# Kernel optimization log

Hardware: AMD Instinct MI355X
Metric: run time of the kernel (lower is better)

## Reference

```python
import jax, jax.numpy as jnp
import numpy as np

EPS = 1e-5

def _conv1x1(x, w, b):
    # x: (b,c,t,h,w), w: (o,c), b: (o,)  -> (b,o,t,h,w)
    return jnp.einsum('bcthw,oc->bothw', x, w) + b[None, :, None, None, None]

def setup_inputs() -> dict:
    key = jax.random.key(0)
    ks = jax.random.split(key, 12)
    B, C, IC, T, H, W = 32, 1024, 512, 8, 16, 8
    s_c = 1.0 / np.sqrt(C)
    s_ic = 1.0 / np.sqrt(IC)
    return {
        'x':       jax.random.normal(ks[0], (B, C, T, H, W), jnp.float32),
        'g_w':     jax.random.normal(ks[1], (IC, C), jnp.float32) * s_c,
        'g_b':     jax.random.normal(ks[2], (IC,), jnp.float32) * 0.01,
        'theta_w': jax.random.normal(ks[3], (IC, C), jnp.float32) * s_c,
        'theta_b': jax.random.normal(ks[4], (IC,), jnp.float32) * 0.01,
        'phi_w':   jax.random.normal(ks[5], (IC, C), jnp.float32) * s_c,
        'phi_b':   jax.random.normal(ks[6], (IC,), jnp.float32) * 0.01,
        'w_w':     jax.random.normal(ks[7], (C, IC), jnp.float32) * s_ic,
        'w_b':     jax.random.normal(ks[8], (C,), jnp.float32) * 0.01,
        'bn_gamma': jax.random.normal(ks[9], (C,), jnp.float32) * 0.1 + 1.0,
        'bn_beta':  jax.random.normal(ks[10], (C,), jnp.float32) * 0.01,
        'bn_mean':  jax.random.normal(ks[11], (C,), jnp.float32) * 0.01,
        'bn_var':   jnp.ones((C,), jnp.float32),
    }

def reference(x, g_w, g_b, theta_w, theta_b, phi_w, phi_b, w_w, w_b,
              bn_gamma, bn_beta, bn_mean, bn_var):
    B, C, T, H, W = x.shape
    IC = g_w.shape[0]
    # value projection, flattened per frame: (b, t, ic*h*w)
    g_x = _conv1x1(x, g_w, g_b)                       # (b,ic,t,h,w)
    g_x = jnp.transpose(g_x, (0, 2, 1, 3, 4)).reshape(B, T, IC * H * W)
    # pooled query/key over spatial dims: (b,t,ic) and (b,ic,t)
    theta = _conv1x1(x, theta_w, theta_b).mean(axis=(3, 4))   # (b,ic,t)
    phi = _conv1x1(x, phi_w, phi_b).mean(axis=(3, 4))         # (b,ic,t)
    f = jnp.einsum('bct,bcs->bts', theta, phi)                # (b,t,t)
    attn = jax.nn.softmax(f, axis=-1)
    y = jnp.einsum('bts,bsd->btd', attn, g_x)                 # (b,t,ic*h*w)
    y = jnp.transpose(y.reshape(B, T, IC, H, W), (0, 2, 1, 3, 4))  # (b,ic,t,h,w)
    # output projection + BatchNorm3d (inference stats) + residual
    wy = _conv1x1(y, w_w, w_b)                        # (b,c,t,h,w)
    inv = bn_gamma / jnp.sqrt(bn_var + EPS)
    wy = wy * inv[None, :, None, None, None] + (bn_beta - bn_mean * inv)[None, :, None, None, None]
    return wy + x
```

## Files before the change

kernel.cpp:

```cpp
#include <hip/hip_runtime.h>
#include <hip/hip_bf16.h>

typedef __attribute__((ext_vector_type(8))) short bf16x8;
typedef __attribute__((ext_vector_type(4))) float f32x4;

__global__ __launch_bounds__(256) void pool_kernel(const float* __restrict__ x,
                                                   float* __restrict__ xbar) {
    int row = blockIdx.x * 16 + (threadIdx.x >> 4);
    int j = threadIdx.x & 15;
    const float4* p = (const float4*)(x + (size_t)row * 128);
    float4 a = p[j * 2], b2 = p[j * 2 + 1];
    float s = a.x + a.y + a.z + a.w + b2.x + b2.y + b2.z + b2.w;
    s += __shfl_xor(s, 1); s += __shfl_xor(s, 2);
    s += __shfl_xor(s, 4); s += __shfl_xor(s, 8);
    if (j == 0) xbar[row] = s * (1.0f / 128.0f);
}

__global__ __launch_bounds__(256) void thetaphi_kernel(
        const float* __restrict__ xbar,
        const float* __restrict__ tw, const float* __restrict__ tb,
        const float* __restrict__ pw, const float* __restrict__ pb,
        float* __restrict__ theta, float* __restrict__ phi) {
    int which = blockIdx.x & 1;
    int icc = (blockIdx.x >> 1) & 15;
    int b = blockIdx.x >> 5;
    const float* w = which ? pw : tw;
    const float* bias = which ? pb : tb;
    float* out = which ? phi : theta;
    __shared__ float xs[8192];
    for (int i = threadIdx.x; i < 8192; i += 256) xs[i] = xbar[b * 8192 + i];
    __syncthreads();
    int icl = threadIdx.x >> 3;
    int t = threadIdx.x & 7;
    int ic = icc * 32 + icl;
    const float* wr = w + (size_t)ic * 1024;
    float acc = 0.0f;
    #pragma unroll 8
    for (int k = 0; k < 1024; k++) acc += wr[k] * xs[k * 8 + t];
    out[((size_t)b * 512 + ic) * 8 + t] = acc + bias[ic];
}

__global__ __launch_bounds__(64) void attn_kernel(const float* __restrict__ theta,
                                                  const float* __restrict__ phi,
                                                  float* __restrict__ attn) {
    __shared__ float th[4096], ph[4096];
    int b = blockIdx.x, lane = threadIdx.x;
    for (int i = lane; i < 4096; i += 64) {
        th[i] = theta[(size_t)b * 4096 + i];
        ph[i] = phi[(size_t)b * 4096 + i];
    }
    __syncthreads();
    int t = lane >> 3, s = lane & 7;
    float f = 0.0f;
    #pragma unroll 8
    for (int ic = 0; ic < 512; ic++) f += th[ic * 8 + t] * ph[ic * 8 + s];
    float m = f;
    m = fmaxf(m, __shfl_xor(m, 1));
    m = fmaxf(m, __shfl_xor(m, 2));
    m = fmaxf(m, __shfl_xor(m, 4));
    float e = __expf(f - m);
    float sum = e;
    sum += __shfl_xor(sum, 1); sum += __shfl_xor(sum, 2); sum += __shfl_xor(sum, 4);
    attn[b * 64 + lane] = e / sum;
}

__global__ __launch_bounds__(256) void prep_operands_kernel(
        const float* __restrict__ gw, const float* __restrict__ ww,
        __hip_bfloat16* __restrict__ gwt, __hip_bfloat16* __restrict__ wwb) {
    int bid = blockIdx.x;
    if (bid < 512) {
        int icb = bid >> 5;
        int cb = bid & 31;
        __shared__ float tile[32][33];
        int r = threadIdx.x >> 5, c = threadIdx.x & 31;
        #pragma unroll
        for (int i = 0; i < 4; i++)
            tile[r + i * 8][c] = gw[(size_t)(icb * 32 + r + i * 8) * 1024 + cb * 32 + c];
        __syncthreads();
        #pragma unroll
        for (int i = 0; i < 4; i++) {
            int cin = cb * 32 + r + i * 8;
            gwt[(size_t)cin * 512 + icb * 32 + c] = __float2bfloat16(tile[c][r + i * 8]);
        }
    } else {
        int b2 = bid - 512;
        size_t base = (size_t)b2 * 2048 + (size_t)threadIdx.x * 8;
        const float4* src = (const float4*)(ww + base);
        float4 v0 = src[0], v1 = src[1];
        __hip_bfloat16 tmp[8];
        tmp[0] = __float2bfloat16(v0.x); tmp[1] = __float2bfloat16(v0.y);
        tmp[2] = __float2bfloat16(v0.z); tmp[3] = __float2bfloat16(v0.w);
        tmp[4] = __float2bfloat16(v1.x); tmp[5] = __float2bfloat16(v1.y);
        tmp[6] = __float2bfloat16(v1.z); tmp[7] = __float2bfloat16(v1.w);
        *(bf16x8*)(wwb + base) = *(const bf16x8*)tmp;
    }
}

#if defined(__has_builtin)
#if __has_builtin(__builtin_amdgcn_global_load_lds)
#define USE_GLOAD_LDS 1
#endif
#endif

__device__ __forceinline__ void gload_lds16(const void* g, void* ldsbase) {
#ifdef USE_GLOAD_LDS
    __builtin_amdgcn_global_load_lds(
        (__attribute__((address_space(1))) void*)(g),
        (__attribute__((address_space(3))) void*)(ldsbase), 16, 0, 0);
#endif
}

__global__ __launch_bounds__(256) void prepM_mfma_kernel(
        const __hip_bfloat16* __restrict__ wwb,
        const __hip_bfloat16* __restrict__ gwt,
        __hip_bfloat16* __restrict__ M) {
    __shared__ __align__(16) __hip_bfloat16 As[128 * 32];
    __shared__ __align__(16) __hip_bfloat16 Bs[128 * 32];
    int bid = blockIdx.x;
    int mb = bid >> 3, nb = bid & 7;
    int c0 = mb * 128, n0 = nb * 128;
    int tid = threadIdx.x;
    int w = tid >> 6, l = tid & 63;
    int wr = w >> 1, wc = w & 1;
    const __hip_bfloat16* Ab = wwb + (size_t)c0 * 512;
    const __hip_bfloat16* Bb = gwt + (size_t)n0 * 512;
    int arow = tid >> 2, akq = tid & 3;
    f32x4 acc[4][4] = {};

    for (int kk = 0; kk < 16; ++kk) {
        int k0 = kk * 32;
#ifdef USE_GLOAD_LDS
        gload_lds16(Ab + (size_t)arow * 512 + k0 + akq * 8,        (char*)As + w * 1024);
        gload_lds16(Ab + (size_t)(arow + 64) * 512 + k0 + akq * 8, (char*)As + 4096 + w * 1024);
        gload_lds16(Bb + (size_t)arow * 512 + k0 + akq * 8,        (char*)Bs + w * 1024);
        gload_lds16(Bb + (size_t)(arow + 64) * 512 + k0 + akq * 8, (char*)Bs + 4096 + w * 1024);
#else
        *(bf16x8*)((char*)As + (size_t)tid * 16)        = *(const bf16x8*)(Ab + (size_t)arow * 512 + k0 + akq * 8);
        *(bf16x8*)((char*)As + 4096 + (size_t)tid * 16) = *(const bf16x8*)(Ab + (size_t)(arow + 64) * 512 + k0 + akq * 8);
        *(bf16x8*)((char*)Bs + (size_t)tid * 16)        = *(const bf16x8*)(Bb + (size_t)arow * 512 + k0 + akq * 8);
        *(bf16x8*)((char*)Bs + 4096 + (size_t)tid * 16) = *(const bf16x8*)(Bb + (size_t)(arow + 64) * 512 + k0 + akq * 8);
#endif
        __syncthreads();
        const __hip_bfloat16* Ap = As + ((size_t)(wr * 64 + (l & 15)) * 32) + (l >> 4) * 8;
        const __hip_bfloat16* Bp = Bs + ((size_t)(wc * 64 + (l & 15)) * 32) + (l >> 4) * 8;
        bf16x8 af[4], bfr[4];
        #pragma unroll
        for (int m = 0; m < 4; m++) af[m] = *(const bf16x8*)(Ap + m * 16 * 32);
        #pragma unroll
        for (int n = 0; n < 4; n++) bfr[n] = *(const bf16x8*)(Bp + n * 16 * 32);
        #pragma unroll
        for (int m = 0; m < 4; m++)
            #pragma unroll
            for (int n = 0; n < 4; n++)
                acc[m][n] = __builtin_amdgcn_mfma_f32_16x16x32_bf16(af[m], bfr[n], acc[m][n], 0, 0, 0);
        __syncthreads();
    }

    int col = l & 15, rg = l >> 4;
    #pragma unroll
    for (int m = 0; m < 4; m++)
        #pragma unroll
        for (int j = 0; j < 4; j++) {
            int gc = c0 + wr * 64 + m * 16 + rg * 4 + j;
            #pragma unroll
            for (int n = 0; n < 4; n++)
                M[(size_t)gc * 1024 + n0 + wc * 64 + n * 16 + col] = __float2bfloat16(acc[m][n][j]);
        }
}

__global__ __launch_bounds__(256) void prepbias_kernel(
        const float* __restrict__ ww, const float* __restrict__ gb,
        const float* __restrict__ wb, const float* __restrict__ gamma,
        const float* __restrict__ beta, const float* __restrict__ mean,
        const float* __restrict__ var, float* __restrict__ inv,
        float* __restrict__ shift) {
    int wv = threadIdx.x >> 6, l = threadIdx.x & 63;
    int c = blockIdx.x * 32 + wv * 8 + (l >> 3);
    int j = l & 7;
    const float* wr = ww + (size_t)c * 512;
    float acc = 0.0f;
    #pragma unroll 8
    for (int k = j; k < 512; k += 8) acc += wr[k] * gb[k];
    acc += __shfl_xor(acc, 1); acc += __shfl_xor(acc, 2); acc += __shfl_xor(acc, 4);
    if (j == 0) {
        float cb = wb[c] + acc;
        float iv = gamma[c] * rsqrtf(var[c] + 1e-5f);
        inv[c] = iv;
        shift[c] = cb * iv + beta[c] - mean[c] * iv;
    }
}

__global__ __launch_bounds__(256) void mix_kernel(const float* __restrict__ x,
                                                  const float* __restrict__ attn,
                                                  __hip_bfloat16* __restrict__ xmt) {
    int orig = blockIdx.x;
    int wg = (orig & 7) * 64 + (orig >> 3);
    int b = wg >> 4;
    int hwg = wg & 15;
    __shared__ float at[64];
    __shared__ float xs[8][8][33];
    int tid = threadIdx.x;
    if (tid < 64) at[tid] = attn[b * 64 + tid];
    int ci = tid >> 3, s = tid & 7;
    int h = tid >> 5, cq = tid & 31;
    const float* xb = x + ((size_t)b << 20);
    __hip_bfloat16* ob = xmt + ((size_t)b << 20);
    for (int cc = 0; cc < 32; ++cc) {
        const float4* src = (const float4*)(xb + ((size_t)(cc * 32 + ci) * 8 + s) * 128 + hwg * 8);
        float4 v0 = src[0], v1 = src[1];
        __syncthreads();
        xs[s][0][ci] = v0.x; xs[s][1][ci] = v0.y; xs[s][2][ci] = v0.z; xs[s][3][ci] = v0.w;
        xs[s][4][ci] = v1.x; xs[s][5][ci] = v1.y; xs[s][6][ci] = v1.z; xs[s][7][ci] = v1.w;
        __syncthreads();
        float xr[8];
        #pragma unroll
        for (int ss = 0; ss < 8; ss++) xr[ss] = xs[ss][h][cq];
        #pragma unroll
        for (int t = 0; t < 8; t++) {
            float o = 0.0f;
            #pragma unroll
            for (int ss = 0; ss < 8; ss++) o += at[t * 8 + ss] * xr[ss];
            ob[(size_t)(t * 128 + hwg * 8 + h) * 1024 + cc * 32 + cq] = __float2bfloat16(o);
        }
    }
}

__global__ __launch_bounds__(512, 2) void gemm256_kernel(
        const __hip_bfloat16* __restrict__ Mw,
        const __hip_bfloat16* __restrict__ xmt,
        const float* __restrict__ x,
        const float* __restrict__ inv, const float* __restrict__ shift,
        float* __restrict__ out) {
    __shared__ __align__(16) __hip_bfloat16 HBs[65536];
    char* AH = (char*)HBs;
    const int BUFB = 32768;

    int orig = blockIdx.x;
    int bid = (orig & 7) * 64 + (orig >> 3);
    int b = bid >> 4;
    int mb = (bid >> 2) & 3;
    int nb = bid & 3;
    int c0 = mb * 256, n0 = nb * 256;

    int tid = threadIdx.x;
    int w = tid >> 6, l = tid & 63;
    int wr = w >> 2, wc = w & 3;

    int sgl = (((l & 3) - ((l >> 3) & 3)) & 3);
    const __hip_bfloat16* aS = Mw + (size_t)(c0 + w * 16 + (l >> 2)) * 1024 + sgl * 8;
    const __hip_bfloat16* bS = xmt + ((size_t)b << 20) + (size_t)(n0 + w * 16 + (l >> 2)) * 1024 + sgl * 8;
    int stBase = w * 1024;

    int rdSlot = ((l >> 4) + (((l & 15) >> 1) & 3)) & 3;
    int aRdBase = (wr * 128 + (l & 15)) * 64 + rdSlot * 16;
    int bRdBase = 16384 + (wc * 64 + (l & 15)) * 64 + rdSlot * 16;

    f32x4 acc[8][4] = {};

    #define ISSUE(q3) do {                                                      \
        gload_lds16(aS,              AH + (q3) * BUFB + stBase);                \
        gload_lds16(aS + 128 * 1024, AH + (q3) * BUFB + stBase + 8192);         \
        gload_lds16(bS,              AH + (q3) * BUFB + 16384 + stBase);        \
        gload_lds16(bS + 128 * 1024, AH + (q3) * BUFB + 16384 + stBase + 8192); \
        aS += 32; bS += 32;                                                     \
    } while (0)

    #define V8 asm volatile("s_waitcnt vmcnt(8)" ::: "memory")
    #define V4 asm volatile("s_waitcnt vmcnt(4)" ::: "memory")
    #define V0 asm volatile("s_waitcnt vmcnt(0)" ::: "memory")

    #define HSTEP(q, DOISS, WAITM, LAST) do {                                   \
        if (DOISS) ISSUE(((q) + 3) & 3);                                        \
        const char* bufA = AH + (q) * BUFB;                                     \
        bf16x8 bfr[4];                                                          \
        _Pragma("unroll")                                                       \
        for (int n = 0; n < 4; ++n)                                             \
            bfr[n] = *(const bf16x8*)(bufA + bRdBase + n * 1024);               \
        __builtin_amdgcn_s_setprio(1);                                          \
        _Pragma("unroll")                                                       \
        for (int mi = 0; mi < 8; ++mi) {                                        \
            bf16x8 af = *(const bf16x8*)(bufA + aRdBase + mi * 1024);           \
            _Pragma("unroll")                                                   \
            for (int n = 0; n < 4; ++n)                                         \
                acc[mi][n] = __builtin_amdgcn_mfma_f32_16x16x32_bf16(           \
                    af, bfr[n], acc[mi][n], 0, 0, 0);                           \
        }                                                                       \
        __builtin_amdgcn_s_setprio(0);                                          \
        if (!LAST) {                                                            \
            WAITM;                                                              \
            __builtin_amdgcn_s_barrier();                                       \
            __builtin_amdgcn_sched_barrier(0);                                  \
        }                                                                       \
    } while (0)

    ISSUE(0); ISSUE(1); ISSUE(2);
    V8;
    __builtin_amdgcn_s_barrier();
    __builtin_amdgcn_sched_barrier(0);

    #pragma unroll 1
    for (int t = 0; t < 7; ++t) {
        HSTEP(0, 1, V8, 0);
        HSTEP(1, 1, V8, 0);
        HSTEP(2, 1, V8, 0);
        HSTEP(3, 1, V8, 0);
    }
    HSTEP(0, 1, V8, 0);
    HSTEP(1, 0, V4, 0);
    HSTEP(2, 0, V0, 0);
    HSTEP(3, 0, V0, 1);

    #undef ISSUE
    #undef HSTEP
    #undef V8
    #undef V4
    #undef V0

    int col = l & 15, rg = l >> 4;
    const float* xb = x + ((size_t)b << 20);
    float* ob = out + ((size_t)b << 20);
    #pragma unroll
    for (int mi = 0; mi < 8; ++mi) {
        #pragma unroll
        for (int j = 0; j < 4; ++j) {
            int gc = c0 + wr * 128 + mi * 16 + rg * 4 + j;
            float iv = inv[gc], sh = shift[gc];
            size_t rowoff = (size_t)gc * 1024 + n0 + wc * 64 + col;
            #pragma unroll
            for (int n = 0; n < 4; ++n) {
                size_t idx = rowoff + n * 16;
                ob[idx] = acc[mi][n][j] * iv + sh + xb[idx];
            }
        }
    }
}

extern "C" void kernel_launch(void* const* d_in, const int* in_sizes, int n_in,
                              void* d_out, int out_size, void* d_ws, size_t ws_size,
                              hipStream_t stream) {
    const float* x    = (const float*)d_in[0];
    const float* g_w  = (const float*)d_in[1];
    const float* g_b  = (const float*)d_in[2];
    const float* th_w = (const float*)d_in[3];
    const float* th_b = (const float*)d_in[4];
    const float* ph_w = (const float*)d_in[5];
    const float* ph_b = (const float*)d_in[6];
    const float* w_w  = (const float*)d_in[7];
    const float* w_b  = (const float*)d_in[8];
    const float* gam  = (const float*)d_in[9];
    const float* bet  = (const float*)d_in[10];
    const float* mea  = (const float*)d_in[11];
    const float* var  = (const float*)d_in[12];
    float* out = (float*)d_out;
    char* ws = (char*)d_ws;

    __hip_bfloat16* xmt = (__hip_bfloat16*)ws;
    __hip_bfloat16* Mw  = (__hip_bfloat16*)(ws + 67108864);
    float* xbar  = (float*)(ws + 69206016);
    float* theta = (float*)(ws + 70254592);
    float* phi   = (float*)(ws + 70778880);
    float* attn  = (float*)(ws + 71303168);
    float* inv   = (float*)(ws + 71311360);
    float* shift = (float*)(ws + 71315456);
    __hip_bfloat16* gwt = (__hip_bfloat16*)ws;
    __hip_bfloat16* wwb = (__hip_bfloat16*)(ws + 1048576);

    hipLaunchKernelGGL(pool_kernel, dim3(16384), dim3(256), 0, stream, x, xbar);
    hipLaunchKernelGGL(thetaphi_kernel, dim3(1024), dim3(256), 0, stream,
                       xbar, th_w, th_b, ph_w, ph_b, theta, phi);
    hipLaunchKernelGGL(attn_kernel, dim3(32), dim3(64), 0, stream, theta, phi, attn);
    hipLaunchKernelGGL(prep_operands_kernel, dim3(768), dim3(256), 0, stream,
                       g_w, w_w, gwt, wwb);
    hipLaunchKernelGGL(prepM_mfma_kernel, dim3(64), dim3(256), 0, stream, wwb, gwt, Mw);
    hipLaunchKernelGGL(prepbias_kernel, dim3(32), dim3(256), 0, stream,
                       w_w, g_b, w_b, gam, bet, mea, var, inv, shift);
    hipLaunchKernelGGL(mix_kernel, dim3(512), dim3(256), 0, stream, x, attn, xmt);
    hipLaunchKernelGGL(gemm256_kernel, dim3(512), dim3(512), 0, stream,
                       Mw, xmt, x, inv, shift, out);
}
```

Baseline: 238.2 us.

## Merge independent prep kernels into two combined launches by block-index dispatch

Combines pooling, weight transpose/convert, and bias prep into one early kernel, and the theta/phi projection with the M-weight MFMA GEMM into a second kernel, dispatching on block index. This cuts the launch count from eight to five and lets independent small stages run concurrently on the GPU instead of back to back. The trade-off is larger, uniform shared memory (32 KB) for all blocks of the second kernel, which could lower occupancy for the theta/phi blocks.

```diff
diff --git a/kernel.cpp b/kernel.cpp
--- a/kernel.cpp
+++ b/kernel.cpp
@@ -4,40 +4,163 @@
 typedef __attribute__((ext_vector_type(8))) short bf16x8;
 typedef __attribute__((ext_vector_type(4))) float f32x4;
 
-__global__ __launch_bounds__(256) void pool_kernel(const float* __restrict__ x,
-                                                   float* __restrict__ xbar) {
-    int row = blockIdx.x * 16 + (threadIdx.x >> 4);
-    int j = threadIdx.x & 15;
-    const float4* p = (const float4*)(x + (size_t)row * 128);
-    float4 a = p[j * 2], b2 = p[j * 2 + 1];
-    float s = a.x + a.y + a.z + a.w + b2.x + b2.y + b2.z + b2.w;
-    s += __shfl_xor(s, 1); s += __shfl_xor(s, 2);
-    s += __shfl_xor(s, 4); s += __shfl_xor(s, 8);
-    if (j == 0) xbar[row] = s * (1.0f / 128.0f);
-}
-
-__global__ __launch_bounds__(256) void thetaphi_kernel(
+#if defined(__has_builtin)
+#if __has_builtin(__builtin_amdgcn_global_load_lds)
+#define USE_GLOAD_LDS 1
+#endif
+#endif
+
+__device__ __forceinline__ void gload_lds16(const void* g, void* ldsbase) {
+#ifdef USE_GLOAD_LDS
+    __builtin_amdgcn_global_load_lds(
+        (__attribute__((address_space(1))) void*)(g),
+        (__attribute__((address_space(3))) void*)(ldsbase), 16, 0, 0);
+#endif
+}
+
+__global__ __launch_bounds__(256) void early_kernel(
+        const float* __restrict__ x, float* __restrict__ xbar,
+        const float* __restrict__ gw, const float* __restrict__ ww,
+        __hip_bfloat16* __restrict__ gwt, __hip_bfloat16* __restrict__ wwb,
+        const float* __restrict__ gb, const float* __restrict__ wb,
+        const float* __restrict__ gamma, const float* __restrict__ beta,
+        const float* __restrict__ mean, const float* __restrict__ var,
+        float* __restrict__ inv, float* __restrict__ shift) {
+    __shared__ float tile[32][33];
+    int bid = blockIdx.x;
+    int tid = threadIdx.x;
+    if (bid < 16384) {
+        int row = bid * 16 + (tid >> 4);
+        int j = tid & 15;
+        const float4* p = (const float4*)(x + (size_t)row * 128);
+        float4 a = p[j * 2], b2 = p[j * 2 + 1];
+        float s = a.x + a.y + a.z + a.w + b2.x + b2.y + b2.z + b2.w;
+        s += __shfl_xor(s, 1); s += __shfl_xor(s, 2);
+        s += __shfl_xor(s, 4); s += __shfl_xor(s, 8);
+        if (j == 0) xbar[row] = s * (1.0f / 128.0f);
+    } else if (bid < 16896) {
+        int b2 = bid - 16384;
+        int icb = b2 >> 5, cb = b2 & 31;
+        int r = tid >> 5, c = tid & 31;
+        #pragma unroll
+        for (int i = 0; i < 4; i++)
+            tile[r + i * 8][c] = gw[(size_t)(icb * 32 + r + i * 8) * 1024 + cb * 32 + c];
+        __syncthreads();
+        #pragma unroll
+        for (int i = 0; i < 4; i++) {
+            int cin = cb * 32 + r + i * 8;
+            gwt[(size_t)cin * 512 + icb * 32 + c] = __float2bfloat16(tile[c][r + i * 8]);
+        }
+    } else if (bid < 17152) {
+        int b2 = bid - 16896;
+        size_t base = (size_t)b2 * 2048 + (size_t)tid * 8;
+        const float4* src = (const float4*)(ww + base);
+        float4 v0 = src[0], v1 = src[1];
+        __hip_bfloat16 tmp[8];
+        tmp[0] = __float2bfloat16(v0.x); tmp[1] = __float2bfloat16(v0.y);
+        tmp[2] = __float2bfloat16(v0.z); tmp[3] = __float2bfloat16(v0.w);
+        tmp[4] = __float2bfloat16(v1.x); tmp[5] = __float2bfloat16(v1.y);
+        tmp[6] = __float2bfloat16(v1.z); tmp[7] = __float2bfloat16(v1.w);
+        *(bf16x8*)(wwb + base) = *(const bf16x8*)tmp;
+    } else {
+        int b2 = bid - 17152;
+        int wv = tid >> 6, l = tid & 63;
+        int c = b2 * 32 + wv * 8 + (l >> 3);
+        int j = l & 7;
+        const float* wr = ww + (size_t)c * 512;
+        float acc = 0.0f;
+        #pragma unroll 8
+        for (int k = j; k < 512; k += 8) acc += wr[k] * gb[k];
+        acc += __shfl_xor(acc, 1); acc += __shfl_xor(acc, 2); acc += __shfl_xor(acc, 4);
+        if (j == 0) {
+            float cb2 = wb[c] + acc;
+            float iv = gamma[c] * rsqrtf(var[c] + 1e-5f);
+            inv[c] = iv;
+            shift[c] = cb2 * iv + beta[c] - mean[c] * iv;
+        }
+    }
+}
+
+__global__ __launch_bounds__(256) void stage2_kernel(
         const float* __restrict__ xbar,
         const float* __restrict__ tw, const float* __restrict__ tb,
         const float* __restrict__ pw, const float* __restrict__ pb,
-        float* __restrict__ theta, float* __restrict__ phi) {
-    int which = blockIdx.x & 1;
-    int icc = (blockIdx.x >> 1) & 15;
-    int b = blockIdx.x >> 5;
-    const float* w = which ? pw : tw;
-    const float* bias = which ? pb : tb;
-    float* out = which ? phi : theta;
-    __shared__ float xs[8192];
-    for (int i = threadIdx.x; i < 8192; i += 256) xs[i] = xbar[b * 8192 + i];
-    __syncthreads();
-    int icl = threadIdx.x >> 3;
-    int t = threadIdx.x & 7;
-    int ic = icc * 32 + icl;
-    const float* wr = w + (size_t)ic * 1024;
-    float acc = 0.0f;
-    #pragma unroll 8
-    for (int k = 0; k < 1024; k++) acc += wr[k] * xs[k * 8 + t];
-    out[((size_t)b * 512 + ic) * 8 + t] = acc + bias[ic];
+        float* __restrict__ theta, float* __restrict__ phi,
+        const __hip_bfloat16* __restrict__ wwb,
+        const __hip_bfloat16* __restrict__ gwt,
+        __hip_bfloat16* __restrict__ M) {
+    __shared__ __align__(16) char smem[32768];
+    int bid = blockIdx.x;
+    int tid = threadIdx.x;
+    if (bid < 1024) {
+        float* xs = (float*)smem;
+        int which = bid & 1;
+        int icc = (bid >> 1) & 15;
+        int b = bid >> 5;
+        const float* w = which ? pw : tw;
+        const float* bias = which ? pb : tb;
+        float* out = which ? phi : theta;
+        for (int i = tid; i < 8192; i += 256) xs[i] = xbar[b * 8192 + i];
+        __syncthreads();
+        int icl = tid >> 3;
+        int t = tid & 7;
+        int ic = icc * 32 + icl;
+        const float* wr = w + (size_t)ic * 1024;
+        float acc = 0.0f;
+        #pragma unroll 8
+        for (int k = 0; k < 1024; k++) acc += wr[k] * xs[k * 8 + t];
+        out[((size_t)b * 512 + ic) * 8 + t] = acc + bias[ic];
+    } else {
+        __hip_bfloat16* As = (__hip_bfloat16*)smem;
+        __hip_bfloat16* Bs = (__hip_bfloat16*)(smem + 8192);
+        int b2 = bid - 1024;
+        int mb = b2 >> 3, nb = b2 & 7;
+        int c0 = mb * 128, n0 = nb * 128;
+        int w = tid >> 6, l = tid & 63;
+        int wr = w >> 1, wc = w & 1;
+        const __hip_bfloat16* Ab = wwb + (size_t)c0 * 512;
+        const __hip_bfloat16* Bb = gwt + (size_t)n0 * 512;
+        int arow = tid >> 2, akq = tid & 3;
+        f32x4 acc[4][4] = {};
+        for (int kk = 0; kk < 16; ++kk) {
+            int k0 = kk * 32;
+#ifdef USE_GLOAD_LDS
+            gload_lds16(Ab + (size_t)arow * 512 + k0 + akq * 8,        (char*)As + w * 1024);
+            gload_lds16(Ab + (size_t)(arow + 64) * 512 + k0 + akq * 8, (char*)As + 4096 + w * 1024);
+            gload_lds16(Bb + (size_t)arow * 512 + k0 + akq * 8,        (char*)Bs + w * 1024);
+            gload_lds16(Bb + (size_t)(arow + 64) * 512 + k0 + akq * 8, (char*)Bs + 4096 + w * 1024);
+#else
+            *(bf16x8*)((char*)As + (size_t)tid * 16)        = *(const bf16x8*)(Ab + (size_t)arow * 512 + k0 + akq * 8);
+            *(bf16x8*)((char*)As + 4096 + (size_t)tid * 16) = *(const bf16x8*)(Ab + (size_t)(arow + 64) * 512 + k0 + akq * 8);
+            *(bf16x8*)((char*)Bs + (size_t)tid * 16)        = *(const bf16x8*)(Bb + (size_t)arow * 512 + k0 + akq * 8);
+            *(bf16x8*)((char*)Bs + 4096 + (size_t)tid * 16) = *(const bf16x8*)(Bb + (size_t)(arow + 64) * 512 + k0 + akq * 8);
+#endif
+            __syncthreads();
+            const __hip_bfloat16* Ap = As + ((size_t)(wr * 64 + (l & 15)) * 32) + (l >> 4) * 8;
+            const __hip_bfloat16* Bp = Bs + ((size_t)(wc * 64 + (l & 15)) * 32) + (l >> 4) * 8;
+            bf16x8 af[4], bfr[4];
+            #pragma unroll
+            for (int m = 0; m < 4; m++) af[m] = *(const bf16x8*)(Ap + m * 16 * 32);
+            #pragma unroll
+            for (int n = 0; n < 4; n++) bfr[n] = *(const bf16x8*)(Bp + n * 16 * 32);
+            #pragma unroll
+            for (int m = 0; m < 4; m++)
+                #pragma unroll
+                for (int n = 0; n < 4; n++)
+                    acc[m][n] = __builtin_amdgcn_mfma_f32_16x16x32_bf16(af[m], bfr[n], acc[m][n], 0, 0, 0);
+            __syncthreads();
+        }
+        int col = l & 15, rg = l >> 4;
+        #pragma unroll
+        for (int m = 0; m < 4; m++)
+            #pragma unroll
+            for (int j = 0; j < 4; j++) {
+                int gc = c0 + wr * 64 + m * 16 + rg * 4 + j;
+                #pragma unroll
+                for (int n = 0; n < 4; n++)
+                    M[(size_t)gc * 1024 + n0 + wc * 64 + n * 16 + col] = __float2bfloat16(acc[m][n][j]);
+            }
+    }
 }
 
 __global__ __launch_bounds__(64) void attn_kernel(const float* __restrict__ theta,
@@ -62,132 +185,6 @@
     float sum = e;
     sum += __shfl_xor(sum, 1); sum += __shfl_xor(sum, 2); sum += __shfl_xor(sum, 4);
     attn[b * 64 + lane] = e / sum;
-}
-
-__global__ __launch_bounds__(256) void prep_operands_kernel(
-        const float* __restrict__ gw, const float* __restrict__ ww,
-        __hip_bfloat16* __restrict__ gwt, __hip_bfloat16* __restrict__ wwb) {
-    int bid = blockIdx.x;
-    if (bid < 512) {
-        int icb = bid >> 5;
-        int cb = bid & 31;
-        __shared__ float tile[32][33];
-        int r = threadIdx.x >> 5, c = threadIdx.x & 31;
-        #pragma unroll
-        for (int i = 0; i < 4; i++)
-            tile[r + i * 8][c] = gw[(size_t)(icb * 32 + r + i * 8) * 1024 + cb * 32 + c];
-        __syncthreads();
-        #pragma unroll
-        for (int i = 0; i < 4; i++) {
-            int cin = cb * 32 + r + i * 8;
-            gwt[(size_t)cin * 512 + icb * 32 + c] = __float2bfloat16(tile[c][r + i * 8]);
-        }
-    } else {
-        int b2 = bid - 512;
-        size_t base = (size_t)b2 * 2048 + (size_t)threadIdx.x * 8;
-        const float4* src = (const float4*)(ww + base);
-        float4 v0 = src[0], v1 = src[1];
-        __hip_bfloat16 tmp[8];
-        tmp[0] = __float2bfloat16(v0.x); tmp[1] = __float2bfloat16(v0.y);
-        tmp[2] = __float2bfloat16(v0.z); tmp[3] = __float2bfloat16(v0.w);
-        tmp[4] = __float2bfloat16(v1.x); tmp[5] = __float2bfloat16(v1.y);
-        tmp[6] = __float2bfloat16(v1.z); tmp[7] = __float2bfloat16(v1.w);
-        *(bf16x8*)(wwb + base) = *(const bf16x8*)tmp;
-    }
-}
-
-#if defined(__has_builtin)
-#if __has_builtin(__builtin_amdgcn_global_load_lds)
-#define USE_GLOAD_LDS 1
-#endif
-#endif
-
-__device__ __forceinline__ void gload_lds16(const void* g, void* ldsbase) {
-#ifdef USE_GLOAD_LDS
-    __builtin_amdgcn_global_load_lds(
-        (__attribute__((address_space(1))) void*)(g),
-        (__attribute__((address_space(3))) void*)(ldsbase), 16, 0, 0);
-#endif
-}
-
-__global__ __launch_bounds__(256) void prepM_mfma_kernel(
-        const __hip_bfloat16* __restrict__ wwb,
-        const __hip_bfloat16* __restrict__ gwt,
-        __hip_bfloat16* __restrict__ M) {
-    __shared__ __align__(16) __hip_bfloat16 As[128 * 32];
-    __shared__ __align__(16) __hip_bfloat16 Bs[128 * 32];
-    int bid = blockIdx.x;
-    int mb = bid >> 3, nb = bid & 7;
-    int c0 = mb * 128, n0 = nb * 128;
-    int tid = threadIdx.x;
-    int w = tid >> 6, l = tid & 63;
-    int wr = w >> 1, wc = w & 1;
-    const __hip_bfloat16* Ab = wwb + (size_t)c0 * 512;
-    const __hip_bfloat16* Bb = gwt + (size_t)n0 * 512;
-    int arow = tid >> 2, akq = tid & 3;
-    f32x4 acc[4][4] = {};
-
-    for (int kk = 0; kk < 16; ++kk) {
-        int k0 = kk * 32;
-#ifdef USE_GLOAD_LDS
-        gload_lds16(Ab + (size_t)arow * 512 + k0 + akq * 8,        (char*)As + w * 1024);
-        gload_lds16(Ab + (size_t)(arow + 64) * 512 + k0 + akq * 8, (char*)As + 4096 + w * 1024);
-        gload_lds16(Bb + (size_t)arow * 512 + k0 + akq * 8,        (char*)Bs + w * 1024);
-        gload_lds16(Bb + (size_t)(arow + 64) * 512 + k0 + akq * 8, (char*)Bs + 4096 + w * 1024);
-#else
-        *(bf16x8*)((char*)As + (size_t)tid * 16)        = *(const bf16x8*)(Ab + (size_t)arow * 512 + k0 + akq * 8);
-        *(bf16x8*)((char*)As + 4096 + (size_t)tid * 16) = *(const bf16x8*)(Ab + (size_t)(arow + 64) * 512 + k0 + akq * 8);
-        *(bf16x8*)((char*)Bs + (size_t)tid * 16)        = *(const bf16x8*)(Bb + (size_t)arow * 512 + k0 + akq * 8);
-        *(bf16x8*)((char*)Bs + 4096 + (size_t)tid * 16) = *(const bf16x8*)(Bb + (size_t)(arow + 64) * 512 + k0 + akq * 8);
-#endif
-        __syncthreads();
-        const __hip_bfloat16* Ap = As + ((size_t)(wr * 64 + (l & 15)) * 32) + (l >> 4) * 8;
-        const __hip_bfloat16* Bp = Bs + ((size_t)(wc * 64 + (l & 15)) * 32) + (l >> 4) * 8;
-        bf16x8 af[4], bfr[4];
-        #pragma unroll
-        for (int m = 0; m < 4; m++) af[m] = *(const bf16x8*)(Ap + m * 16 * 32);
-        #pragma unroll
-        for (int n = 0; n < 4; n++) bfr[n] = *(const bf16x8*)(Bp + n * 16 * 32);
-        #pragma unroll
-        for (int m = 0; m < 4; m++)
-            #pragma unroll
-            for (int n = 0; n < 4; n++)
-                acc[m][n] = __builtin_amdgcn_mfma_f32_16x16x32_bf16(af[m], bfr[n], acc[m][n], 0, 0, 0);
-        __syncthreads();
-    }
-
-    int col = l & 15, rg = l >> 4;
-    #pragma unroll
-    for (int m = 0; m < 4; m++)
-        #pragma unroll
-        for (int j = 0; j < 4; j++) {
-            int gc = c0 + wr * 64 + m * 16 + rg * 4 + j;
-            #pragma unroll
-            for (int n = 0; n < 4; n++)
-                M[(size_t)gc * 1024 + n0 + wc * 64 + n * 16 + col] = __float2bfloat16(acc[m][n][j]);
-        }
-}
-
-__global__ __launch_bounds__(256) void prepbias_kernel(
-        const float* __restrict__ ww, const float* __restrict__ gb,
-        const float* __restrict__ wb, const float* __restrict__ gamma,
-        const float* __restrict__ beta, const float* __restrict__ mean,
-        const float* __restrict__ var, float* __restrict__ inv,
-        float* __restrict__ shift) {
-    int wv = threadIdx.x >> 6, l = threadIdx.x & 63;
-    int c = blockIdx.x * 32 + wv * 8 + (l >> 3);
-    int j = l & 7;
-    const float* wr = ww + (size_t)c * 512;
-    float acc = 0.0f;
-    #pragma unroll 8
-    for (int k = j; k < 512; k += 8) acc += wr[k] * gb[k];
-    acc += __shfl_xor(acc, 1); acc += __shfl_xor(acc, 2); acc += __shfl_xor(acc, 4);
-    if (j == 0) {
-        float cb = wb[c] + acc;
-        float iv = gamma[c] * rsqrtf(var[c] + 1e-5f);
-        inv[c] = iv;
-        shift[c] = cb * iv + beta[c] - mean[c] * iv;
-    }
 }
 
 __global__ __launch_bounds__(256) void mix_kernel(const float* __restrict__ x,
@@ -365,15 +362,12 @@
     __hip_bfloat16* gwt = (__hip_bfloat16*)ws;
     __hip_bfloat16* wwb = (__hip_bfloat16*)(ws + 1048576);
 
-    hipLaunchKernelGGL(pool_kernel, dim3(16384), dim3(256), 0, stream, x, xbar);
-    hipLaunchKernelGGL(thetaphi_kernel, dim3(1024), dim3(256), 0, stream,
-                       xbar, th_w, th_b, ph_w, ph_b, theta, phi);
+    hipLaunchKernelGGL(early_kernel, dim3(17184), dim3(256), 0, stream,
+                       x, xbar, g_w, w_w, gwt, wwb,
+                       g_b, w_b, gam, bet, mea, var, inv, shift);
+    hipLaunchKernelGGL(stage2_kernel, dim3(1088), dim3(256), 0, stream,
+                       xbar, th_w, th_b, ph_w, ph_b, theta, phi, wwb, gwt, Mw);
     hipLaunchKernelGGL(attn_kernel, dim3(32), dim3(64), 0, stream, theta, phi, attn);
-    hipLaunchKernelGGL(prep_operands_kernel, dim3(768), dim3(256), 0, stream,
-                       g_w, w_w, gwt, wwb);
-    hipLaunchKernelGGL(prepM_mfma_kernel, dim3(64), dim3(256), 0, stream, wwb, gwt, Mw);
-    hipLaunchKernelGGL(prepbias_kernel, dim3(32), dim3(256), 0, stream,
-                       w_w, g_b, w_b, gam, bet, mea, var, inv, shift);
     hipLaunchKernelGGL(mix_kernel, dim3(512), dim3(256), 0, stream, x, attn, xmt);
     hipLaunchKernelGGL(gemm256_kernel, dim3(512), dim3(512), 0, stream,
                        Mw, xmt, x, inv, shift, out);
```

Result: no change. 236.7 us (-0.7%).
